# Kernel optimization log

Hardware: AMD Instinct MI355X
Metric: run time of the kernel (lower is better)

Reference implementation:

```python
import jax, jax.numpy as jnp
import numpy as np

GRID = 128
N = GRID * GRID  # number of torus nodes, node id v = x + GRID * y
HID = 64
OUT = 1
BATCH = 64


def _neighbor_idx():
    # Replicates gen_neighbor_lists: sparse matrices are permutation gathers
    # (A x)[v] = x[neighbor(v)] on a periodic grid.
    idx = np.arange(N)
    xc = idx % GRID
    yc = idx // GRID
    up = xc + ((yc + 1) % GRID) * GRID
    down = xc + ((yc - 1) % GRID) * GRID
    left = (xc - 1) % GRID + yc * GRID
    right = (xc + 1) % GRID + yc * GRID
    return np.stack([up, down, left, right], axis=0).astype(np.int32)  # [4, N]

NBR = jnp.asarray(_neighbor_idx())


def setup_inputs() -> dict:
    key = jax.random.key(0)
    ks = jax.random.split(key, 7)
    s4, sh = 1.0 / np.sqrt(4.0), 1.0 / np.sqrt(HID)
    return {
        "x": jax.random.normal(ks[0], (BATCH, N, 2), dtype=jnp.float32),
        "H": jnp.eye(2, dtype=jnp.float32),
        "W_emb": jax.random.uniform(ks[1], (4, HID), jnp.float32, -s4, s4),
        "b_emb": jax.random.uniform(ks[2], (HID,), jnp.float32, -s4, s4),
        "W_hid": jax.random.uniform(ks[3], (HID, HID), jnp.float32, -sh, sh),
        "b_hid": jax.random.uniform(ks[4], (HID,), jnp.float32, -sh, sh),
        "W_post": jax.random.uniform(ks[5], (HID, OUT), jnp.float32, -sh, sh),
        "b_post": jax.random.uniform(ks[6], (OUT,), jnp.float32, -sh, sh),
    }


def reference(x, H, W_emb, b_emb, W_hid, b_hid, W_post, b_post):
    # Permutation-matrix sparse.mm == direct neighbor gather: [B, 4, N, 2]
    xn = x[:, NBR, :]
    # Bilinear form per direction/node: s[b,i,k] = sum_{m,n} x[b,i,m] H[m,n] xn[b,k,i,n]
    s = jnp.einsum('bim,bkin,mn->bik', x, xn, H)  # [B, N, 4]
    h = jax.nn.relu(s @ W_emb + b_emb)            # [B, N, HID]
    h = jax.nn.relu(h @ W_hid + b_hid)            # [B, N, HID]
    h = h @ W_post + b_post                       # [B, N, OUT]
    return h.sum(axis=1)                          # [B, OUT]
```

## Files before the change

kernel.cpp:

```cpp
#include <hip/hip_runtime.h>
#include <hip/hip_bf16.h>

#define GRID_D 128
#define NSITES (GRID_D * GRID_D)
#define HID 64
#define BATCH 64

#define WPB 4
#define BLOCKS 4096
#define BLOCKS_PER_BATCH (BLOCKS / BATCH)
#define WAVES_TOTAL (BLOCKS * WPB)
#define WAVES_PER_BATCH (WAVES_TOTAL / BATCH)
#define TILES_PER_WAVE (NSITES / (WAVES_PER_BATCH * 16))

typedef short bf16x8 __attribute__((ext_vector_type(8)));
typedef float f32x4  __attribute__((ext_vector_type(4)));

__device__ __forceinline__ unsigned short f2bf(float f) {
    return __builtin_bit_cast(unsigned short, __float2bfloat16(f));
}

__global__ __launch_bounds__(256)
void gauge_mfma(const float* __restrict__ x,
                const float* __restrict__ H,
                const float* __restrict__ W_emb,
                const float* __restrict__ b_emb,
                const float* __restrict__ W_hid,
                const float* __restrict__ b_hid,
                const float* __restrict__ W_post,
                float* __restrict__ ws)
{
    const int tid   = threadIdx.x;
    const int lane  = tid & 63;
    const int widx  = tid >> 6;
    const int wgid  = blockIdx.x * WPB + widx;
    const int b     = wgid / WAVES_PER_BATCH;
    const int wslot = wgid % WAVES_PER_BATCH;

    const int ls = lane & 15;
    const int kl = (lane >> 4) * 8;

    const float h00 = H[0], h01 = H[1], h10 = H[2], h11 = H[3];

    bf16x8 bfrag[4][2];
    #pragma unroll
    for (int t = 0; t < 4; ++t) {
        #pragma unroll
        for (int s = 0; s < 2; ++s) {
            union { bf16x8 v; unsigned short us[8]; } r;
            #pragma unroll
            for (int i = 0; i < 8; ++i)
                r.us[i] = f2bf(W_hid[(s * 32 + kl + i) * HID + t * 16 + ls]);
            bfrag[t][s] = r.v;
        }
    }

    float bh[4], wp[4];
    #pragma unroll
    for (int t = 0; t < 4; ++t) {
        bh[t] = b_hid[t * 16 + ls];
        wp[t] = W_post[t * 16 + ls];
    }

    float be[2][8];
    #pragma unroll
    for (int s = 0; s < 2; ++s) {
        const float4 v0 = *(const float4*)(b_emb + s * 32 + kl);
        const float4 v1 = *(const float4*)(b_emb + s * 32 + kl + 4);
        be[s][0] = v0.x; be[s][1] = v0.y; be[s][2] = v0.z; be[s][3] = v0.w;
        be[s][4] = v1.x; be[s][5] = v1.y; be[s][6] = v1.z; be[s][7] = v1.w;
    }

    const float* __restrict__ xb = x + (size_t)b * NSITES * 2;
    const int wbase = wslot * (16 * TILES_PER_WAVE);
    float o = 0.0f;

    for (int tile = 0; tile < TILES_PER_WAVE; ++tile) {
        const int site = wbase + tile * 16 + ls;
        const int xc = site & (GRID_D - 1);
        const int yc = site >> 7;
        const int n0 = xc + (((yc + 1) & (GRID_D - 1)) << 7);
        const int n1 = xc + (((yc - 1) & (GRID_D - 1)) << 7);
        const int n2 = ((xc - 1) & (GRID_D - 1)) + (yc << 7);
        const int n3 = ((xc + 1) & (GRID_D - 1)) + (yc << 7);

        const float2 xi = *(const float2*)(xb + 2 * site);
        const float2 xu = *(const float2*)(xb + 2 * n0);
        const float2 xd = *(const float2*)(xb + 2 * n1);
        const float2 xl = *(const float2*)(xb + 2 * n2);
        const float2 xr = *(const float2*)(xb + 2 * n3);

        const float s0 = xi.x * fmaf(h00, xu.x, h01 * xu.y) + xi.y * fmaf(h10, xu.x, h11 * xu.y);
        const float s1 = xi.x * fmaf(h00, xd.x, h01 * xd.y) + xi.y * fmaf(h10, xd.x, h11 * xd.y);
        const float s2 = xi.x * fmaf(h00, xl.x, h01 * xl.y) + xi.y * fmaf(h10, xl.x, h11 * xl.y);
        const float s3 = xi.x * fmaf(h00, xr.x, h01 * xr.y) + xi.y * fmaf(h10, xr.x, h11 * xr.y);

        bf16x8 afrag[2];
        #pragma unroll
        for (int s = 0; s < 2; ++s) {
            const int kb = s * 32 + kl;
            float hv[8];
            #pragma unroll
            for (int i = 0; i < 8; ++i) hv[i] = be[s][i];
            #pragma unroll
            for (int m = 0; m < 4; ++m) {
                const float sm = (m == 0) ? s0 : (m == 1) ? s1 : (m == 2) ? s2 : s3;
                const float4 w0 = *(const float4*)(W_emb + m * HID + kb);
                const float4 w1 = *(const float4*)(W_emb + m * HID + kb + 4);
                hv[0] = fmaf(sm, w0.x, hv[0]); hv[1] = fmaf(sm, w0.y, hv[1]);
                hv[2] = fmaf(sm, w0.z, hv[2]); hv[3] = fmaf(sm, w0.w, hv[3]);
                hv[4] = fmaf(sm, w1.x, hv[4]); hv[5] = fmaf(sm, w1.y, hv[5]);
                hv[6] = fmaf(sm, w1.z, hv[6]); hv[7] = fmaf(sm, w1.w, hv[7]);
            }
            union { bf16x8 v; unsigned short us[8]; } r;
            #pragma unroll
            for (int i = 0; i < 8; ++i)
                r.us[i] = f2bf(fmaxf(hv[i], 0.0f));
            afrag[s] = r.v;
        }

        #pragma unroll
        for (int t = 0; t < 4; ++t) {
            f32x4 acc = { bh[t], bh[t], bh[t], bh[t] };
            acc = __builtin_amdgcn_mfma_f32_16x16x32_bf16(afrag[0], bfrag[t][0], acc, 0, 0, 0);
            acc = __builtin_amdgcn_mfma_f32_16x16x32_bf16(afrag[1], bfrag[t][1], acc, 0, 0, 0);
            #pragma unroll
            for (int r = 0; r < 4; ++r)
                o = fmaf(fmaxf(acc[r], 0.0f), wp[t], o);
        }
    }

    #pragma unroll
    for (int off = 32; off > 0; off >>= 1)
        o += __shfl_down(o, off, 64);

    __shared__ float part[WPB];
    if (lane == 0) part[widx] = o;
    __syncthreads();
    if (tid == 0)
        ws[blockIdx.x] = part[0] + part[1] + part[2] + part[3];
}

__global__ __launch_bounds__(64)
void gauge_reduce(const float* __restrict__ ws,
                  const float* __restrict__ b_post,
                  float* __restrict__ out)
{
    const int b = threadIdx.x;
    float t = (float)NSITES * b_post[0];
    #pragma unroll
    for (int j = 0; j < BLOCKS_PER_BATCH; ++j)
        t += ws[b * BLOCKS_PER_BATCH + j];
    out[b] = t;
}

extern "C" void kernel_launch(void* const* d_in, const int* in_sizes, int n_in,
                              void* d_out, int out_size, void* d_ws, size_t ws_size,
                              hipStream_t stream)
{
    const float* x      = (const float*)d_in[0];
    const float* H      = (const float*)d_in[1];
    const float* W_emb  = (const float*)d_in[2];
    const float* b_emb  = (const float*)d_in[3];
    const float* W_hid  = (const float*)d_in[4];
    const float* b_hid  = (const float*)d_in[5];
    const float* W_post = (const float*)d_in[6];
    const float* b_post = (const float*)d_in[7];
    float* out = (float*)d_out;
    float* ws  = (float*)d_ws;

    gauge_mfma<<<dim3(BLOCKS), dim3(256), 0, stream>>>(
        x, H, W_emb, b_emb, W_hid, b_hid, W_post, ws);
    gauge_reduce<<<dim3(1), dim3(64), 0, stream>>>(ws, b_post, out);
}
```

Baseline: 111.6 us.

## Compute embedding layer with MFMA and feed its output directly as next A fragment

The first dense layer (4->64 plus bias) now runs on the matrix cores. The bias is folded in through a constant-one input column, and K is zero-padded to 32 across the lane groups. The layer's output registers are repacked with packed bf16 conversion straight into the A fragments of the hidden layer, and the W_hid fragment indexing is permuted to match that layout. This removes the per-lane scalar FMA chain and the W_emb loads inside the tile loop, at the cost of four mostly-zero MFMAs per tile. The block count is also halved so each wave processes more tiles.

```diff
diff --git a/kernel.cpp b/kernel.cpp
--- a/kernel.cpp
+++ b/kernel.cpp
@@ -7,10 +7,9 @@
 #define BATCH 64
 
 #define WPB 4
-#define BLOCKS 4096
+#define BLOCKS 2048
 #define BLOCKS_PER_BATCH (BLOCKS / BATCH)
-#define WAVES_TOTAL (BLOCKS * WPB)
-#define WAVES_PER_BATCH (WAVES_TOTAL / BATCH)
+#define WAVES_PER_BATCH (BLOCKS_PER_BATCH * WPB)
 #define TILES_PER_WAVE (NSITES / (WAVES_PER_BATCH * 16))
 
 typedef short bf16x8 __attribute__((ext_vector_type(8)));
@@ -19,6 +18,14 @@
 __device__ __forceinline__ unsigned short f2bf(float f) {
     return __builtin_bit_cast(unsigned short, __float2bfloat16(f));
 }
+
+__device__ __forceinline__ unsigned cvt_pk_bf16(float a, float b) {
+    unsigned r;
+    asm("v_cvt_pk_bf16_f32 %0, %1, %2" : "=v"(r) : "v"(a), "v"(b));
+    return r;
+}
+
+union frag_u { bf16x8 v; unsigned u[4]; unsigned short us[8]; };
 
 __global__ __launch_bounds__(256)
 void gauge_mfma(const float* __restrict__ x,
@@ -37,8 +44,9 @@
     const int b     = wgid / WAVES_PER_BATCH;
     const int wslot = wgid % WAVES_PER_BATCH;
 
-    const int ls = lane & 15;
-    const int kl = (lane >> 4) * 8;
+    const int  ls  = lane & 15;
+    const int  kg  = lane >> 4;
+    const bool kg0 = (kg == 0);
 
     const float h00 = H[0], h01 = H[1], h10 = H[2], h11 = H[3];
 
@@ -47,12 +55,31 @@
     for (int t = 0; t < 4; ++t) {
         #pragma unroll
         for (int s = 0; s < 2; ++s) {
-            union { bf16x8 v; unsigned short us[8]; } r;
+            frag_u r;
             #pragma unroll
-            for (int i = 0; i < 8; ++i)
-                r.us[i] = f2bf(W_hid[(s * 32 + kl + i) * HID + t * 16 + ls]);
+            for (int i = 0; i < 8; ++i) {
+                const int khid = s * 32 + ((i & 4) << 2) + (kg << 2) + (i & 3);
+                r.us[i] = f2bf(W_hid[khid * HID + t * 16 + ls]);
+            }
             bfrag[t][s] = r.v;
         }
+    }
+
+    bf16x8 afe[4];
+    #pragma unroll
+    for (int m = 0; m < 4; ++m) {
+        const int col = m * 16 + ls;
+        const float w0 = W_emb[0 * HID + col];
+        const float w1 = W_emb[1 * HID + col];
+        const float w2 = W_emb[2 * HID + col];
+        const float w3 = W_emb[3 * HID + col];
+        const float bb = b_emb[col];
+        frag_u r;
+        r.u[0] = kg0 ? cvt_pk_bf16(w0, w1) : 0u;
+        r.u[1] = kg0 ? cvt_pk_bf16(w2, w3) : 0u;
+        r.u[2] = kg0 ? (unsigned)f2bf(bb) : 0u;
+        r.u[3] = 0u;
+        afe[m] = r.v;
     }
 
     float bh[4], wp[4];
@@ -62,17 +89,9 @@
         wp[t] = W_post[t * 16 + ls];
     }
 
-    float be[2][8];
-    #pragma unroll
-    for (int s = 0; s < 2; ++s) {
-        const float4 v0 = *(const float4*)(b_emb + s * 32 + kl);
-        const float4 v1 = *(const float4*)(b_emb + s * 32 + kl + 4);
-        be[s][0] = v0.x; be[s][1] = v0.y; be[s][2] = v0.z; be[s][3] = v0.w;
-        be[s][4] = v1.x; be[s][5] = v1.y; be[s][6] = v1.z; be[s][7] = v1.w;
-    }
-
     const float* __restrict__ xb = x + (size_t)b * NSITES * 2;
     const int wbase = wslot * (16 * TILES_PER_WAVE);
+    const unsigned sd2 = kg0 ? 0x00003F80u : 0u;
     float o = 0.0f;
 
     for (int tile = 0; tile < TILES_PER_WAVE; ++tile) {
@@ -95,35 +114,45 @@
         const float s2 = xi.x * fmaf(h00, xl.x, h01 * xl.y) + xi.y * fmaf(h10, xl.x, h11 * xl.y);
         const float s3 = xi.x * fmaf(h00, xr.x, h01 * xr.y) + xi.y * fmaf(h10, xr.x, h11 * xr.y);
 
-        bf16x8 afrag[2];
+        frag_u bs;
+        const unsigned p01 = cvt_pk_bf16(s0, s1);
+        const unsigned p23 = cvt_pk_bf16(s2, s3);
+        bs.u[0] = kg0 ? p01 : 0u;
+        bs.u[1] = kg0 ? p23 : 0u;
+        bs.u[2] = sd2;
+        bs.u[3] = 0u;
+
+        f32x4 D0 = {0.f, 0.f, 0.f, 0.f};
+        f32x4 D1 = {0.f, 0.f, 0.f, 0.f};
+        f32x4 D2 = {0.f, 0.f, 0.f, 0.f};
+        f32x4 D3 = {0.f, 0.f, 0.f, 0.f};
+        D0 = __builtin_amdgcn_mfma_f32_16x16x32_bf16(afe[0], bs.v, D0, 0, 0, 0);
+        D1 = __builtin_amdgcn_mfma_f32_16x16x32_bf16(afe[1], bs.v, D1, 0, 0, 0);
+        D2 = __builtin_amdgcn_mfma_f32_16x16x32_bf16(afe[2], bs.v, D2, 0, 0, 0);
+        D3 = __builtin_amdgcn_mfma_f32_16x16x32_bf16(afe[3], bs.v, D3, 0, 0, 0);
+
         #pragma unroll
-        for (int s = 0; s < 2; ++s) {
-            const int kb = s * 32 + kl;
-            float hv[8];
-            #pragma unroll
-            for (int i = 0; i < 8; ++i) hv[i] = be[s][i];
-            #pragma unroll
-            for (int m = 0; m < 4; ++m) {
-                const float sm = (m == 0) ? s0 : (m == 1) ? s1 : (m == 2) ? s2 : s3;
-                const float4 w0 = *(const float4*)(W_emb + m * HID + kb);
-                const float4 w1 = *(const float4*)(W_emb + m * HID + kb + 4);
-                hv[0] = fmaf(sm, w0.x, hv[0]); hv[1] = fmaf(sm, w0.y, hv[1]);
-                hv[2] = fmaf(sm, w0.z, hv[2]); hv[3] = fmaf(sm, w0.w, hv[3]);
-                hv[4] = fmaf(sm, w1.x, hv[4]); hv[5] = fmaf(sm, w1.y, hv[5]);
-                hv[6] = fmaf(sm, w1.z, hv[6]); hv[7] = fmaf(sm, w1.w, hv[7]);
-            }
-            union { bf16x8 v; unsigned short us[8]; } r;
-            #pragma unroll
-            for (int i = 0; i < 8; ++i)
-                r.us[i] = f2bf(fmaxf(hv[i], 0.0f));
-            afrag[s] = r.v;
+        for (int r = 0; r < 4; ++r) {
+            D0[r] = fmaxf(D0[r], 0.0f);
+            D1[r] = fmaxf(D1[r], 0.0f);
+            D2[r] = fmaxf(D2[r], 0.0f);
+            D3[r] = fmaxf(D3[r], 0.0f);
         }
+        frag_u ah0, ah1;
+        ah0.u[0] = cvt_pk_bf16(D0[0], D0[1]);
+        ah0.u[1] = cvt_pk_bf16(D0[2], D0[3]);
+        ah0.u[2] = cvt_pk_bf16(D1[0], D1[1]);
+        ah0.u[3] = cvt_pk_bf16(D1[2], D1[3]);
+        ah1.u[0] = cvt_pk_bf16(D2[0], D2[1]);
+        ah1.u[1] = cvt_pk_bf16(D2[2], D2[3]);
+        ah1.u[2] = cvt_pk_bf16(D3[0], D3[1]);
+        ah1.u[3] = cvt_pk_bf16(D3[2], D3[3]);
 
         #pragma unroll
         for (int t = 0; t < 4; ++t) {
             f32x4 acc = { bh[t], bh[t], bh[t], bh[t] };
-            acc = __builtin_amdgcn_mfma_f32_16x16x32_bf16(afrag[0], bfrag[t][0], acc, 0, 0, 0);
-            acc = __builtin_amdgcn_mfma_f32_16x16x32_bf16(afrag[1], bfrag[t][1], acc, 0, 0, 0);
+            acc = __builtin_amdgcn_mfma_f32_16x16x32_bf16(ah0.v, bfrag[t][0], acc, 0, 0, 0);
+            acc = __builtin_amdgcn_mfma_f32_16x16x32_bf16(ah1.v, bfrag[t][1], acc, 0, 0, 0);
             #pragma unroll
             for (int r = 0; r < 4; ++r)
                 o = fmaf(fmaxf(acc[r], 0.0f), wp[t], o);
```

New measurement: 97.05 us. 13.0% less time.
